# Optimization experiments

Hardware: AMD Instinct MI355X
Metric: run time of the kernel (lower is better)

The kernel has to match this reference:

```python
import jax, jax.numpy as jnp
import numpy as np
from jax import lax

L = 12  # db6 filter length
REC_LO = np.array([0.11154074335008017, 0.4946238903983854, 0.7511339080215775,
                   0.3152503517092432, -0.22626469396516913, -0.12976686756709563,
                   0.09750160558707936, 0.02752286553001629, -0.031582039318031156,
                   0.0005538422009938016, 0.004777257511010651, -0.00107730108499558])
DEC_LO = REC_LO[::-1]
_sgn = (-1.0) ** np.arange(L)
DEC_HI = -_sgn * REC_LO            # pywt dec_hi
REC_HI = _sgn * DEC_LO             # pywt rec_hi
# XLA conv = cross-correlation; pytorch_wavelets correlates with reversed dec filters
K_ANA = np.ascontiguousarray(np.stack([DEC_LO[::-1], DEC_HI[::-1]])[:, None, :])  # (2,1,12)
# conv_transpose(stride2, pad L-2) == dilate-by-2, pad 1, correlate with flipped rec filters
K_SYN = np.ascontiguousarray(np.stack([REC_LO[::-1], REC_HI[::-1]])[None, :, :])  # (1,2,12)
J = 8


def _afb(x):
    # one analysis level, symmetric mode (pytorch_wavelets afb1d)
    B, C, N = x.shape
    out = (N + L - 1) // 2
    p = 2 * (out - 1) - N + L
    xp = jnp.pad(x, ((0, 0), (0, 0), (p // 2, p - p // 2)), mode='symmetric')
    y = lax.conv_general_dilated(xp.reshape(B * C, 1, -1), jnp.asarray(K_ANA, x.dtype),
                                 (2,), 'VALID', dimension_numbers=('NCH', 'OIH', 'NCH'))
    y = y.reshape(B, C, 2, out)
    return y[:, :, 0], y[:, :, 1]


def _sfb(lo, hi):
    # one synthesis level (pytorch_wavelets sfb1d); crop lo to hi length first
    lo = lo[..., :hi.shape[-1]]
    B, C, N = lo.shape
    z = jnp.stack([lo, hi], 2).reshape(B * C, 2, N)
    y = lax.conv_general_dilated(z, jnp.asarray(K_SYN, lo.dtype), (1,), [(1, 1)],
                                 lhs_dilation=(2,), dimension_numbers=('NCH', 'OIH', 'NCH'))
    return y.reshape(B, C, -1)  # length 2N - L + 2


def _wave_conv(x, w1, w2):
    lo, highs = x, []
    for _ in range(J):
        lo, hi = _afb(lo)
        highs.append(hi)
    lo = jnp.einsum('bix,iox->box', lo, w1)
    highs[-1] = jnp.einsum('bix,iox->box', highs[-1], w2)
    for hi in highs[::-1]:
        lo = _sfb(lo, hi)
    return lo


def _branch(xg, fc0_w, fc0_b, ww1, ww2, cw, cb, fc1_w, fc1_b, fc2_w, fc2_b):
    v = jnp.transpose(xg @ fc0_w + fc0_b, (0, 2, 1))  # (B,C,S)
    for i in range(4):
        a = _wave_conv(v, ww1[i], ww2[i])
        b = jnp.einsum('bcs,oc->bos', v, cw[i]) + cb[i][None, :, None]
        v = a + b
        if i < 3:
            v = jax.nn.gelu(v, approximate=False)
    v = jnp.transpose(v, (0, 2, 1))
    v = jax.nn.gelu(v @ fc1_w + fc1_b, approximate=False)
    return v @ fc2_w + fc2_b


def setup_inputs() -> dict:
    key = jax.random.key(0)
    ks = iter(jax.random.split(key, 32))
    B, S, W, LV = 64, 1024, 64, 8
    d = {"x": jax.random.normal(next(ks), (B, S, 1), jnp.float32)}
    def params(pref):
        sc = 1.0 / (W * W)
        d[pref + "fc0_w"] = jax.random.normal(next(ks), (2, W), jnp.float32) * 0.5
        d[pref + "fc0_b"] = jax.random.normal(next(ks), (W,), jnp.float32) * 0.1
        d[pref + "wave_w1"] = sc * jax.random.uniform(next(ks), (4, W, W, LV + 6), jnp.float32)
        d[pref + "wave_w2"] = sc * jax.random.uniform(next(ks), (4, W, W, LV + 6), jnp.float32)
        d[pref + "cw"] = jax.random.normal(next(ks), (4, W, W), jnp.float32) * (1.0 / np.sqrt(W))
        d[pref + "cb"] = jax.random.normal(next(ks), (4, W), jnp.float32) * 0.05
        d[pref + "fc1_w"] = jax.random.normal(next(ks), (W, 128), jnp.float32) * (1.0 / np.sqrt(W))
        d[pref + "fc1_b"] = jax.random.normal(next(ks), (128,), jnp.float32) * 0.05
        d[pref + "fc2_w"] = jax.random.normal(next(ks), (128, 1), jnp.float32) * (1.0 / np.sqrt(128))
        d[pref + "fc2_b"] = jax.random.normal(next(ks), (1,), jnp.float32) * 0.05
    params("")
    params("nt_")
    return d


def reference(x, fc0_w, fc0_b, wave_w1, wave_w2, cw, cb, fc1_w, fc1_b, fc2_w, fc2_b,
              nt_fc0_w, nt_fc0_b, nt_wave_w1, nt_wave_w2, nt_cw, nt_cb,
              nt_fc1_w, nt_fc1_b, nt_fc2_w, nt_fc2_b):
    B, S, _ = x.shape
    grid = jnp.broadcast_to(jnp.linspace(0.0, 1.0, S, dtype=x.dtype)[None, :, None], (B, S, 1))
    xg = jnp.concatenate([x, grid], -1)
    y = _branch(xg, fc0_w, fc0_b, wave_w1, wave_w2, cw, cb, fc1_w, fc1_b, fc2_w, fc2_b)
    y_nt = _branch(xg, nt_fc0_w, nt_fc0_b, nt_wave_w1, nt_wave_w2, nt_cw, nt_cb,
                   nt_fc1_w, nt_fc1_b, nt_fc2_w, nt_fc2_b)
    return y + y_nt
```

## Files before the change

kernel.cpp:

```cpp
#include <hip/hip_runtime.h>
#include <hip/hip_bf16.h>
#include <math.h>


#define BDIM 64
#define SLEN 1024
#define WCH  64
#define BC   (BDIM*WCH)
#define NT   16

typedef short s16x8 __attribute__((ext_vector_type(8)));
typedef float f32x4 __attribute__((ext_vector_type(4)));
typedef unsigned short u16x4 __attribute__((ext_vector_type(4)));

constexpr float RLv[12] = {
    0.11154074335008017f, 0.4946238903983854f, 0.7511339080215775f,
    0.3152503517092432f, -0.22626469396516913f, -0.12976686756709563f,
    0.09750160558707936f, 0.02752286553001629f, -0.031582039318031156f,
    0.0005538422009938016f, 0.004777257511010651f, -0.00107730108499558f };
constexpr float AHv[12] = {
     RLv[11], -RLv[10],  RLv[9], -RLv[8],  RLv[7], -RLv[6],
     RLv[5],  -RLv[4],   RLv[3], -RLv[2],  RLv[1], -RLv[0] };
constexpr float SLv[12] = {
     RLv[11], RLv[10], RLv[9], RLv[8], RLv[7], RLv[6],
     RLv[5],  RLv[4],  RLv[3], RLv[2], RLv[1], RLv[0] };
constexpr float SHv[12] = {
    -RLv[0],  RLv[1], -RLv[2],  RLv[3], -RLv[4],  RLv[5],
    -RLv[6],  RLv[7], -RLv[8],  RLv[9], -RLv[10], RLv[11] };

__device__ __forceinline__ float gelu_f(float x) {
    float z = 0.7978845608f * (x + 0.044715f * x * x * x);
    return x / (1.0f + __expf(-2.0f * z));
}
__device__ __forceinline__ unsigned short f2bf(float f) {
    __hip_bfloat16 h = __float2bfloat16(f);
    union { __hip_bfloat16 h; unsigned short u; } cv; cv.h = h; return cv.u;
}
__device__ __forceinline__ float bf2f(unsigned short u) {
    union { unsigned short u; __hip_bfloat16 h; } cv; cv.u = u;
    return __bfloat162float(cv.h);
}
__device__ __forceinline__ void unpack_frag2(uint4 a, uint4 b,
                                             s16x8* ah, s16x8* al) {
    union { s16x8 v; unsigned int d[4]; } H, L;
    H.d[0] = __builtin_amdgcn_perm(a.y, a.x, 0x05040100u);
    H.d[1] = __builtin_amdgcn_perm(a.w, a.z, 0x05040100u);
    H.d[2] = __builtin_amdgcn_perm(b.y, b.x, 0x05040100u);
    H.d[3] = __builtin_amdgcn_perm(b.w, b.z, 0x05040100u);
    L.d[0] = __builtin_amdgcn_perm(a.y, a.x, 0x07060302u);
    L.d[1] = __builtin_amdgcn_perm(a.w, a.z, 0x07060302u);
    L.d[2] = __builtin_amdgcn_perm(b.y, b.x, 0x07060302u);
    L.d[3] = __builtin_amdgcn_perm(b.w, b.z, 0x07060302u);
    *ah = H.v; *al = L.v;
}

__device__ __forceinline__ int swz(int c, int s) {
    return c * 64 + ((((s >> 3) ^ (c & 7)) << 3) | (s & 7));
}
__device__ __forceinline__ int swz2(int s, int c) {
    return s * 64 + ((((c >> 3) ^ (s & 7)) << 3) | (c & 7));
}

__device__ __forceinline__ void proj2(
    const unsigned short* Phi, const unsigned short* Plo,
    const unsigned short* __restrict__ Ahi, const unsigned short* __restrict__ Alo,
    float* __restrict__ Ppart, int bb, int tile, int s0, int t)
{
    const int lane = t & 63;
    const int w    = t >> 6;
    const int qr   = lane >> 4;
    const int ln   = lane & 15;

    s16x8 pah[2][2], pal[2][2];
#pragma unroll
    for (int kk = 0; kk < 2; ++kk)
#pragma unroll
        for (int mt = 0; mt < 2; ++mt) {
            const int arow = (mt * 16 + ln) * SLEN + s0 + kk * 32 + qr * 8;
            pah[kk][mt] = *(const s16x8*)&Ahi[arow];
            pal[kk][mt] = *(const s16x8*)&Alo[arow];
        }

    f32x4 pP[2][2], pS[2][2];
#pragma unroll
    for (int mt = 0; mt < 2; ++mt)
#pragma unroll
        for (int ni = 0; ni < 2; ++ni) {
            pP[mt][ni] = (f32x4){0.f,0.f,0.f,0.f};
            pS[mt][ni] = (f32x4){0.f,0.f,0.f,0.f};
        }

#pragma unroll
    for (int kk = 0; kk < 2; ++kk) {
        const int bk = kk * 4 + qr;
#pragma unroll
        for (int ni = 0; ni < 2; ++ni) {
            const int c = w * 32 + ni * 16 + ln;
            const int boff = c * 64 + ((bk ^ (c & 7)) << 3);
            s16x8 bh = *(const s16x8*)&Phi[boff];
            s16x8 bl = *(const s16x8*)&Plo[boff];
#pragma unroll
            for (int mt = 0; mt < 2; ++mt) {
                pP[mt][ni] = __builtin_amdgcn_mfma_f32_16x16x32_bf16(pah[kk][mt], bh, pP[mt][ni], 0, 0, 0);
                pS[mt][ni] = __builtin_amdgcn_mfma_f32_16x16x32_bf16(pal[kk][mt], bh, pS[mt][ni], 0, 0, 0);
                pS[mt][ni] = __builtin_amdgcn_mfma_f32_16x16x32_bf16(pah[kk][mt], bl, pS[mt][ni], 0, 0, 0);
            }
        }
    }
#pragma unroll
    for (int mt = 0; mt < 2; ++mt)
#pragma unroll
        for (int ni = 0; ni < 2; ++ni) {
            const int c = w * 32 + ni * 16 + ln;
            f32x4 pv = pP[mt][ni] + pS[mt][ni];
#pragma unroll
            for (int r = 0; r < 4; ++r) {
                const int xr = mt * 16 + qr * 4 + r;
                if (xr < 28)
                    Ppart[((size_t)(bb * NT + tile) * 28 + xr) * 64 + c] = pv[r];
            }
        }
}

__global__ __launch_bounds__(256) void setup_kernel(
    const float* __restrict__ x,
    unsigned short* __restrict__ Ahi, unsigned short* __restrict__ Alo,
    unsigned short* __restrict__ MThi, unsigned short* __restrict__ MTlo,
    float* __restrict__ axbuf,
    const float* __restrict__ fc1w_0, const float* __restrict__ fc1w_1,
    const float* __restrict__ cw_0, const float* __restrict__ cw_1,
    const float* __restrict__ w1_0, const float* __restrict__ w2_0,
    const float* __restrict__ w1_1, const float* __restrict__ w2_1,
    unsigned short* __restrict__ w1hi, unsigned short* __restrict__ w1lo,
    unsigned short* __restrict__ cwPhi, unsigned short* __restrict__ cwPlo,
    unsigned short* __restrict__ Dhi,  unsigned short* __restrict__ Dlo,
    float* __restrict__ WsT)
{
    __shared__ float Af[1024];
    __shared__ float Bff[520];
    __shared__ float hib[14];
    const int t = threadIdx.x;

    if (blockIdx.x < 1024 || (blockIdx.x >= 1052 && blockIdx.x < 1118)) {
        const bool isA = (blockIdx.x < 1024);
        const int s0 = blockIdx.x;
        const int di = blockIdx.x - 1052;
        for (int i = t; i < SLEN; i += 256) {
            float v;
            if (isA)           v = (i == s0) ? 1.0f : 0.0f;
            else if (di < 64)  v = x[di * SLEN + i];
            else if (di == 64) v = (float)i * (1.0f / 1023.0f);
            else               v = 1.0f;
            Af[i] = v;
        }
        __syncthreads();

        const int NIN[8]  = {1024, 517, 264, 137, 74, 42, 26, 18};
        const int NOUT[8] = { 517, 264, 137,  74, 42, 26, 18, 14};
#pragma unroll
        for (int lev = 0; lev < 8; ++lev) {
            float* in  = (lev & 1) ? Bff : Af;
            float* out = (lev & 1) ? Af : Bff;
            const int nin = NIN[lev], nout = NOUT[lev];
            for (int m = t; m < nout; m += 256) {
                float alo = 0.f, ahi = 0.f;
#pragma unroll
                for (int tt = 0; tt < 12; ++tt) {
                    int jj = 2 * m + tt - 10;
                    if (jj < 0)         jj = -1 - jj;
                    else if (jj >= nin) jj = 2 * nin - 1 - jj;
                    float xv = in[jj];
                    alo += xv * RLv[tt];
                    if (lev == 7) ahi += xv * AHv[tt];
                }
                out[m] = alo;
                if (lev == 7) {
                    if (isA) {
                        unsigned short h1 = f2bf(alo);
                        Ahi[m * SLEN + s0] = h1;
                        Alo[m * SLEN + s0] = f2bf(alo - bf2f(h1));
                        unsigned short h2 = f2bf(ahi);
                        Ahi[(14 + m) * SLEN + s0] = h2;
                        Alo[(14 + m) * SLEN + s0] = f2bf(ahi - bf2f(h2));
                    } else {
                        axbuf[di * 28 + m]      = alo;
                        axbuf[di * 28 + 14 + m] = ahi;
                    }
                }
            }
            __syncthreads();
        }
        if (isA && t < 4) {
            Ahi[(28 + t) * SLEN + s0] = 0; Alo[(28 + t) * SLEN + s0] = 0;
            MThi[s0 * 32 + 28 + t] = 0;    MTlo[s0 * 32 + 28 + t] = 0;
        }
        return;
    }

    if (blockIdx.x >= 1126) {
        const int wsb = blockIdx.x - 1126;
        const int L = wsb >> 2, br = (wsb >> 1) & 1, which = wsb & 1;
        const float* src = (which ? (br ? w2_1 : w2_0) : (br ? w1_1 : w1_0))
                         + (size_t)L * 64 * 64 * 14;
        const size_t dbase = ((size_t)(L * 2 + br) * 28 + which * 14) * 4096;
        for (int e = t; e < 4096; e += 256) {
            const float* sp = src + (size_t)e * 14;
            float v[14];
#pragma unroll
            for (int xi = 0; xi < 14; ++xi) v[xi] = sp[xi];
#pragma unroll
            for (int xi = 0; xi < 14; ++xi)
                WsT[dbase + (size_t)xi * 4096 + e] = v[xi];
        }
        return;
    }

    if (blockIdx.x >= 1118) {
        const int gid = (blockIdx.x - 1118) * 256 + t;
        for (int idx = gid; idx < 16384; idx += 2048) {
            int br = idx >> 13, r = idx & 8191;
            int h = r >> 6, c = r & 63;
            float f = (br ? fc1w_1 : fc1w_0)[c * 128 + h];
            unsigned short hh = f2bf(f);
            w1hi[idx] = hh;
            w1lo[idx] = f2bf(f - bf2f(hh));
        }
        for (int idx = gid; idx < 32768; idx += 2048) {
            int L = idx >> 13, br = (idx >> 12) & 1, e = idx & 4095;
            int k = e >> 6, o = e & 63;
            float val = (br ? cw_1 : cw_0)[(size_t)L * 4096 + o * 64 + k]
                      + ((k == o) ? 1.0f : 0.0f);
            unsigned short h = f2bf(val);
            const int off = (L * 2 + br) * 4096 + o * 64 + k;
            cwPhi[off] = h;
            cwPlo[off] = f2bf(val - bf2f(h));
        }
        for (int idx = gid; idx < 32768; idx += 2048) {
            int bb = idx >> 8, o = (idx >> 2) & 63, j = idx & 3;
            Dhi[bb * 2048 + o * 32 + 28 + j] = 0;
            Dlo[bb * 2048 + o * 32 + 28 + j] = 0;
        }
        return;
    }

    const int u = blockIdx.x - 1024;
    if (t < 14) {
        Af[t]  = (u < 14 && t == u) ? 1.0f : 0.0f;
        hib[t] = (u >= 14 && t == (u - 14)) ? 1.0f : 0.0f;
    }
    __syncthreads();

    const int NH[8] = {14, 18, 26, 42, 74, 137, 264, 517};
    const int NO[8] = {18, 26, 42, 74, 138, 264, 518, 1024};

#pragma unroll
    for (int s = 0; s < 8; ++s) {
        const float* lo = (s & 1) ? Bff : Af;
        float* out      = (s & 1) ? Af : Bff;
        const int N = NH[s], nout = NO[s];
        for (int m = t; m < nout; m += 256) {
            float acc = 0.f;
#pragma unroll
            for (int tt = 0; tt < 12; ++tt) {
                int uu = m + tt - 1;
                if ((uu & 1) == 0) {
                    int q = uu >> 1;
                    if (q < N) {
                        acc += lo[q] * SLv[tt];
                        if (s == 0) acc += hib[q] * SHv[tt];
                    }
                }
            }
            out[m] = acc;
        }
        __syncthreads();
    }
    for (int m = t; m < SLEN; m += 256) {
        float f = Af[m];
        unsigned short h = f2bf(f);
        MThi[m * 32 + u] = h;
        MTlo[m * 32 + u] = f2bf(f - bf2f(h));
    }
}

__global__ __launch_bounds__(256) void mix0_kernel(
    const float* __restrict__ axbuf,
    const float* __restrict__ fc0w_0, const float* __restrict__ fc0b_0,
    const float* __restrict__ fc0w_1, const float* __restrict__ fc0b_1,
    const float* __restrict__ WsT0,
    unsigned short* __restrict__ Dhi, unsigned short* __restrict__ Dlo)
{
    const int t = threadIdx.x;
    const int br  = blockIdx.x / 224;
    const int sub = blockIdx.x % 224;

    __shared__ float Ws[64][65];
    __shared__ float LO[8][64];
    const int o = t & 63;
    const int w = t >> 6;
    const int x  = sub >> 3;
    const int b0 = (sub & 7) << 3;

    const float* wsrc = WsT0 + ((size_t)(br * 28 + x)) * 4096;
    for (int idx = t; idx < 4096; idx += 256)
        Ws[idx >> 6][idx & 63] = wsrc[idx];

    const float* fc0w = br ? fc0w_1 : fc0w_0;
    const float* fc0b = br ? fc0b_1 : fc0b_0;
    const float agv = axbuf[64 * 28 + x];
    const float a1v = axbuf[65 * 28 + x];
    const float w0o = fc0w[o];
    const float wgo = fc0w[WCH + o];
    const float b0o = fc0b[o];

#pragma unroll
    for (int j = 0; j < 2; ++j) {
        int bi = w + 4 * j;
        int b  = b0 + bi;
        float axv = axbuf[b * 28 + x];
        LO[bi][o] = axv * w0o + agv * wgo + a1v * b0o;
    }
    __syncthreads();

#pragma unroll
    for (int j = 0; j < 2; ++j) {
        int bi = w + 4 * j;
        int bb = br * 64 + b0 + bi;
        float acc = 0.f;
        for (int i = 0; i < 64; ++i)
            acc += LO[bi][i] * Ws[i][o];
        acc -= LO[bi][o];
        unsigned short h = f2bf(acc);
        Dhi[bb * 2048 + o * 32 + x] = h;
        Dlo[bb * 2048 + o * 32 + x] = f2bf(acc - bf2f(h));
    }
}

__global__ __launch_bounds__(256) void mix_kernel(
    const float* __restrict__ Ppart,
    const float* __restrict__ WsTL,
    unsigned short* __restrict__ Dhi, unsigned short* __restrict__ Dlo)
{
    const int t = threadIdx.x;
    const int br  = blockIdx.x / 224;
    const int sub = blockIdx.x % 224;

    __shared__ float Ws[64][65];
    __shared__ float LO[8][64];
    const int o = t & 63;
    const int w = t >> 6;
    const int x  = sub >> 3;
    const int b0 = (sub & 7) << 3;

    const float* wsrc = WsTL + ((size_t)(br * 28 + x)) * 4096;
    for (int idx = t; idx < 4096; idx += 256)
        Ws[idx >> 6][idx & 63] = wsrc[idx];

#pragma unroll
    for (int j = 0; j < 2; ++j) {
        int bi = w + 4 * j;
        int bb = br * 64 + b0 + bi;
        float s = 0.f;
        for (int tile = 0; tile < NT; ++tile)
            s += Ppart[((size_t)(bb * NT + tile) * 28 + x) * 64 + o];
        LO[bi][o] = s;
    }
    __syncthreads();

#pragma unroll
    for (int j = 0; j < 2; ++j) {
        int bi = w + 4 * j;
        int bb = br * 64 + b0 + bi;
        float acc = 0.f;
        for (int i = 0; i < 64; ++i)
            acc += LO[bi][i] * Ws[i][o];
        acc -= LO[bi][o];
        unsigned short h = f2bf(acc);
        Dhi[bb * 2048 + o * 32 + x] = h;
        Dlo[bb * 2048 + o * 32 + x] = f2bf(acc - bf2f(h));
    }
}

__global__ __launch_bounds__(128, 3) void layer_kernel(
    const unsigned int* __restrict__ vin0, const unsigned int* __restrict__ vin1,
    unsigned int* __restrict__ vout0, unsigned int* __restrict__ vout1,
    const unsigned short* __restrict__ MThi, const unsigned short* __restrict__ MTlo,
    const unsigned short* __restrict__ Ahi,  const unsigned short* __restrict__ Alo,
    const unsigned short* __restrict__ cwPhi, const unsigned short* __restrict__ cwPlo,
    const unsigned short* __restrict__ Dhi,   const unsigned short* __restrict__ Dlo,
    const float* __restrict__ cb_0, const float* __restrict__ cb_1,
    const float* __restrict__ fc0w_0, const float* __restrict__ fc0b_0,
    const float* __restrict__ fc0w_1, const float* __restrict__ fc0b_1,
    const float* __restrict__ xin,
    float* __restrict__ Ppart, int Lidx)
{
    __shared__ unsigned short Phi[4096];
    __shared__ unsigned short Plo[4096];

    const int t = threadIdx.x;
    const int bid = blockIdx.x;
    const int br  = bid >> 10;
    const int rem = bid & 1023;
    const int b    = rem >> 4;
    const int tile = rem & 15;
    const int s0   = tile << 6;
    const size_t bS = (size_t)b * SLEN;
    const unsigned int* vin = br ? vin1 : vin0;
    unsigned int* vout      = br ? vout1 : vout0;
    const float* cb = br ? cb_1 : cb_0;
    const float* f0w = br ? fc0w_1 : fc0w_0;
    const float* f0b = br ? fc0b_1 : fc0b_0;
    const int bb = br * 64 + b;
    const int cwbase = (Lidx * 2 + br) * 4096;

    const int lane = t & 63;
    const int w    = t >> 6;
    const int qr   = lane >> 4;
    const int ln   = lane & 15;

    s16x8 Bh[2][2], Bl[2][2];
#pragma unroll
    for (int kk = 0; kk < 2; ++kk)
#pragma unroll
        for (int ni = 0; ni < 2; ++ni) {
            const int o = w * 32 + ni * 16 + ln;
            const int boff = cwbase + o * 64 + kk * 32 + qr * 8;
            Bh[kk][ni] = *(const s16x8*)&cwPhi[boff];
            Bl[kk][ni] = *(const s16x8*)&cwPlo[boff];
        }
    s16x8 Dhf[2], Dlf[2];
#pragma unroll
    for (int ni = 0; ni < 2; ++ni) {
        const int o = w * 32 + ni * 16 + ln;
        const int boff = bb * 2048 + o * 32 + qr * 8;
        Dhf[ni] = *(const s16x8*)&Dhi[boff];
        Dlf[ni] = *(const s16x8*)&Dlo[boff];
    }
    float cbv[2];
#pragma unroll
    for (int ni = 0; ni < 2; ++ni) cbv[ni] = cb[w * 32 + ni * 16 + ln];

    uint4 vb[2][2];
    float xpf = 0.f;
    if (Lidx == 0) {
        xpf = xin[bS + s0 + ln];
    } else {
        const size_t a0 = (bS + s0 + ln) * 64 + qr * 8;
        vb[0][0] = *(const uint4*)&vin[a0];
        vb[0][1] = *(const uint4*)&vin[a0 + 4];
        vb[1][0] = *(const uint4*)&vin[a0 + 32];
        vb[1][1] = *(const uint4*)&vin[a0 + 36];
    }

#pragma unroll
    for (int mi = 0; mi < 4; ++mi) {
        const int srow = mi * 16 + ln;
        uint4 vn[2][2];
        float xnf = 0.f;
        if (mi < 3) {
            if (Lidx == 0) {
                xnf = xin[bS + s0 + (mi + 1) * 16 + ln];
            } else {
                const size_t an = (bS + s0 + (mi + 1) * 16 + ln) * 64 + qr * 8;
                vn[0][0] = *(const uint4*)&vin[an];
                vn[0][1] = *(const uint4*)&vin[an + 4];
                vn[1][0] = *(const uint4*)&vin[an + 32];
                vn[1][1] = *(const uint4*)&vin[an + 36];
            }
        }

        f32x4 accP[2], accS[2];
#pragma unroll
        for (int ni = 0; ni < 2; ++ni) {
            accP[ni] = (f32x4){0.f,0.f,0.f,0.f};
            accS[ni] = (f32x4){0.f,0.f,0.f,0.f};
        }

#pragma unroll
        for (int kk = 0; kk < 2; ++kk) {
            s16x8 ah, al;
            if (Lidx == 0) {
                const int s = s0 + srow;
                const float gv = (float)s * (1.0f / 1023.0f);
#pragma unroll
                for (int j = 0; j < 8; ++j) {
                    const int c = kk * 32 + qr * 8 + j;
                    float val = xpf * f0w[c] + gv * f0w[WCH + c] + f0b[c];
                    unsigned short h = f2bf(val);
                    ah[j] = (short)h;
                    al[j] = (short)f2bf(val - bf2f(h));
                }
            } else {
                unpack_frag2(vb[kk][0], vb[kk][1], &ah, &al);
            }
#pragma unroll
            for (int ni = 0; ni < 2; ++ni) {
                accP[ni] = __builtin_amdgcn_mfma_f32_16x16x32_bf16(ah, Bh[kk][ni], accP[ni], 0, 0, 0);
                accS[ni] = __builtin_amdgcn_mfma_f32_16x16x32_bf16(al, Bh[kk][ni], accS[ni], 0, 0, 0);
                accS[ni] = __builtin_amdgcn_mfma_f32_16x16x32_bf16(ah, Bl[kk][ni], accS[ni], 0, 0, 0);
            }
        }
        {
            const size_t aoff = (size_t)(s0 + srow) * 32 + qr * 8;
            s16x8 mh = *(const s16x8*)&MThi[aoff];
            s16x8 ml = *(const s16x8*)&MTlo[aoff];
#pragma unroll
            for (int ni = 0; ni < 2; ++ni) {
                accP[ni] = __builtin_amdgcn_mfma_f32_16x16x32_bf16(mh, Dhf[ni], accP[ni], 0, 0, 0);
                accS[ni] = __builtin_amdgcn_mfma_f32_16x16x32_bf16(ml, Dhf[ni], accS[ni], 0, 0, 0);
                accS[ni] = __builtin_amdgcn_mfma_f32_16x16x32_bf16(mh, Dlf[ni], accS[ni], 0, 0, 0);
            }
        }
#pragma unroll
        for (int ni = 0; ni < 2; ++ni) {
            const int o = w * 32 + ni * 16 + ln;
            f32x4 acc = accP[ni] + accS[ni];
            u16x4 hv, lv;
#pragma unroll
            for (int r = 0; r < 4; ++r) {
                const int sl64 = mi * 16 + qr * 4 + r;
                float val = gelu_f(acc[r] + cbv[ni]);
                unsigned short h = f2bf(val);
                unsigned short l = f2bf(val - bf2f(h));
                vout[(bS + s0 + sl64) * 64 + o] =
                    (unsigned int)h | ((unsigned int)l << 16);
                hv[r] = h;
                lv[r] = l;
            }
            const int a = swz(o, mi * 16 + qr * 4);
            *(u16x4*)&Phi[a] = hv;
            *(u16x4*)&Plo[a] = lv;
        }
        if (mi < 3) {
            if (Lidx == 0) {
                xpf = xnf;
            } else {
                vb[0][0] = vn[0][0]; vb[0][1] = vn[0][1];
                vb[1][0] = vn[1][0]; vb[1][1] = vn[1][1];
            }
        }
    }

    proj2(Phi, Plo, Ahi, Alo, Ppart, bb, tile, s0, t);
}

__global__ __launch_bounds__(256, 2) void head_kernel(
    const unsigned int* __restrict__ vin0, const unsigned int* __restrict__ vin1,
    const unsigned short* __restrict__ MThi, const unsigned short* __restrict__ MTlo,
    const unsigned short* __restrict__ cwPhi, const unsigned short* __restrict__ cwPlo,
    const unsigned short* __restrict__ Dhi,   const unsigned short* __restrict__ Dlo,
    const float* __restrict__ cb_0, const float* __restrict__ cb_1,
    const unsigned short* __restrict__ w1hi, const unsigned short* __restrict__ w1lo,
    const float* __restrict__ fc1b_0, const float* __restrict__ fc2w_0,
    const float* __restrict__ fc2b_0,
    const float* __restrict__ fc1b_1, const float* __restrict__ fc2w_1,
    const float* __restrict__ fc2b_1,
    float* __restrict__ out)
{
    __shared__ unsigned short Vh[8192];
    __shared__ unsigned short Vl[8192];
    __shared__ float SP[4][64];

    const int t = threadIdx.x;
    const int bid = blockIdx.x;
    const int b    = bid >> 4;
    const int tile = bid & 15;
    const int s0   = tile << 6;
    const size_t bS = (size_t)b * SLEN;

    const int lane = t & 63;
    const int w    = t >> 6;
    const int br   = w >> 1;
    const int half = w & 1;
    const int qr   = lane >> 4;
    const int ln   = lane & 15;

    const unsigned int* vin = br ? vin1 : vin0;
    const float* cb   = (br ? cb_1 : cb_0) + 3 * WCH;
    const float* fc1b = br ? fc1b_1 : fc1b_0;
    const float* fc2w = br ? fc2w_1 : fc2w_0;
    const int bb = br * 64 + b;
    const int cwbase = (3 * 2 + br) * 4096;
    unsigned short* Vhp = Vh + br * 4096;
    unsigned short* Vlp = Vl + br * 4096;

    {
        s16x8 Bh[2][2], Bl[2][2];
#pragma unroll
        for (int kk = 0; kk < 2; ++kk)
#pragma unroll
            for (int ni = 0; ni < 2; ++ni) {
                const int o = half * 32 + ni * 16 + ln;
                const int boff = cwbase + o * 64 + kk * 32 + qr * 8;
                Bh[kk][ni] = *(const s16x8*)&cwPhi[boff];
                Bl[kk][ni] = *(const s16x8*)&cwPlo[boff];
            }
        s16x8 Dhf[2], Dlf[2];
#pragma unroll
        for (int ni = 0; ni < 2; ++ni) {
            const int o = half * 32 + ni * 16 + ln;
            const int boff = bb * 2048 + o * 32 + qr * 8;
            Dhf[ni] = *(const s16x8*)&Dhi[boff];
            Dlf[ni] = *(const s16x8*)&Dlo[boff];
        }
        float cbv[2];
#pragma unroll
        for (int ni = 0; ni < 2; ++ni) cbv[ni] = cb[half * 32 + ni * 16 + ln];

        uint4 vb[2][2];
        {
            const size_t a0 = (bS + s0 + ln) * 64 + qr * 8;
            vb[0][0] = *(const uint4*)&vin[a0];
            vb[0][1] = *(const uint4*)&vin[a0 + 4];
            vb[1][0] = *(const uint4*)&vin[a0 + 32];
            vb[1][1] = *(const uint4*)&vin[a0 + 36];
        }

#pragma unroll
        for (int mi = 0; mi < 4; ++mi) {
            uint4 vn[2][2];
            if (mi < 3) {
                const size_t an = (bS + s0 + (mi + 1) * 16 + ln) * 64 + qr * 8;
                vn[0][0] = *(const uint4*)&vin[an];
                vn[0][1] = *(const uint4*)&vin[an + 4];
                vn[1][0] = *(const uint4*)&vin[an + 32];
                vn[1][1] = *(const uint4*)&vin[an + 36];
            }
            const int srow = mi * 16 + ln;
            f32x4 accP[2], accS[2];
#pragma unroll
            for (int ni = 0; ni < 2; ++ni) {
                accP[ni] = (f32x4){0.f,0.f,0.f,0.f};
                accS[ni] = (f32x4){0.f,0.f,0.f,0.f};
            }

#pragma unroll
            for (int kk = 0; kk < 2; ++kk) {
                s16x8 ah, al;
                unpack_frag2(vb[kk][0], vb[kk][1], &ah, &al);
#pragma unroll
                for (int ni = 0; ni < 2; ++ni) {
                    accP[ni] = __builtin_amdgcn_mfma_f32_16x16x32_bf16(ah, Bh[kk][ni], accP[ni], 0, 0, 0);
                    accS[ni] = __builtin_amdgcn_mfma_f32_16x16x32_bf16(al, Bh[kk][ni], accS[ni], 0, 0, 0);
                    accS[ni] = __builtin_amdgcn_mfma_f32_16x16x32_bf16(ah, Bl[kk][ni], accS[ni], 0, 0, 0);
                }
            }
            {
                const size_t aoff = (size_t)(s0 + srow) * 32 + qr * 8;
                s16x8 mh = *(const s16x8*)&MThi[aoff];
                s16x8 ml = *(const s16x8*)&MTlo[aoff];
#pragma unroll
                for (int ni = 0; ni < 2; ++ni) {
                    accP[ni] = __builtin_amdgcn_mfma_f32_16x16x32_bf16(mh, Dhf[ni], accP[ni], 0, 0, 0);
                    accS[ni] = __builtin_amdgcn_mfma_f32_16x16x32_bf16(ml, Dhf[ni], accS[ni], 0, 0, 0);
                    accS[ni] = __builtin_amdgcn_mfma_f32_16x16x32_bf16(mh, Dlf[ni], accS[ni], 0, 0, 0);
                }
            }
#pragma unroll
            for (int ni = 0; ni < 2; ++ni) {
                const int o = half * 32 + ni * 16 + ln;
                f32x4 acc = accP[ni] + accS[ni];
#pragma unroll
                for (int r = 0; r < 4; ++r) {
                    const int sl64 = mi * 16 + qr * 4 + r;
                    float val = acc[r] + cbv[ni];
                    unsigned short h = f2bf(val);
                    unsigned short l = f2bf(val - bf2f(h));
                    const int a = swz2(sl64, o);
                    Vhp[a] = h;
                    Vlp[a] = l;
                }
            }
            if (mi < 3) {
                vb[0][0] = vn[0][0]; vb[0][1] = vn[0][1];
                vb[1][0] = vn[1][0]; vb[1][1] = vn[1][1];
            }
        }
    }
    __syncthreads();

    s16x8 Wh[2][4], Wl[2][4];
#pragma unroll
    for (int kk = 0; kk < 2; ++kk)
#pragma unroll
        for (int ni = 0; ni < 4; ++ni) {
            const int h = half * 64 + ni * 16 + ln;
            const int boff = br * 8192 + h * 64 + kk * 32 + qr * 8;
            Wh[kk][ni] = *(const s16x8*)&w1hi[boff];
            Wl[kk][ni] = *(const s16x8*)&w1lo[boff];
        }
    float b1v[4], w2v[4];
#pragma unroll
    for (int ni = 0; ni < 4; ++ni) {
        b1v[ni] = fc1b[half * 64 + ni * 16 + ln];
        w2v[ni] = fc2w[half * 64 + ni * 16 + ln];
    }

#pragma unroll
    for (int mi = 0; mi < 4; ++mi) {
        f32x4 a1P[4], a1S[4];
#pragma unroll
        for (int ni = 0; ni < 4; ++ni) {
            a1P[ni] = (f32x4){0.f,0.f,0.f,0.f};
            a1S[ni] = (f32x4){0.f,0.f,0.f,0.f};
        }

#pragma unroll
        for (int kk = 0; kk < 2; ++kk) {
            const int blk = kk * 4 + qr;
            const int sl  = mi * 16 + ln;
            const int a   = sl * 64 + ((blk ^ (sl & 7)) << 3);
            s16x8 ah = *(const s16x8*)&Vhp[a];
            s16x8 al = *(const s16x8*)&Vlp[a];
#pragma unroll
            for (int ni = 0; ni < 4; ++ni) {
                a1P[ni] = __builtin_amdgcn_mfma_f32_16x16x32_bf16(ah, Wh[kk][ni], a1P[ni], 0, 0, 0);
                a1S[ni] = __builtin_amdgcn_mfma_f32_16x16x32_bf16(al, Wh[kk][ni], a1S[ni], 0, 0, 0);
                a1S[ni] = __builtin_amdgcn_mfma_f32_16x16x32_bf16(ah, Wl[kk][ni], a1S[ni], 0, 0, 0);
            }
        }
        float partial[4] = {0.f, 0.f, 0.f, 0.f};
#pragma unroll
        for (int ni = 0; ni < 4; ++ni) {
            f32x4 acc1 = a1P[ni] + a1S[ni];
#pragma unroll
            for (int r = 0; r < 4; ++r)
                partial[r] += gelu_f(acc1[r] + b1v[ni]) * w2v[ni];
        }
#pragma unroll
        for (int r = 0; r < 4; ++r) {
            partial[r] += __shfl_xor(partial[r], 1, 64);
            partial[r] += __shfl_xor(partial[r], 2, 64);
            partial[r] += __shfl_xor(partial[r], 4, 64);
            partial[r] += __shfl_xor(partial[r], 8, 64);
        }
        if (ln == 0) {
#pragma unroll
            for (int r = 0; r < 4; ++r)
                SP[w][mi * 16 + qr * 4 + r] = partial[r];
        }
    }
    __syncthreads();

    if (t < 64) {
        const float bias = fc2b_0[0] + fc2b_1[0];
        out[bS + s0 + t] = SP[0][t] + SP[1][t] + SP[2][t] + SP[3][t] + bias;
    }
}

extern "C" void kernel_launch(void* const* d_in, const int* in_sizes, int n_in,
                              void* d_out, int out_size, void* d_ws, size_t ws_size,
                              hipStream_t stream)
{
    const float* x = (const float*)d_in[0];
    const float* P[2][10];
    for (int br = 0; br < 2; ++br)
        for (int k = 0; k < 10; ++k)
            P[br][k] = (const float*)d_in[1 + br * 10 + k];

    char* p = (char*)d_ws;
    const size_t PL = (size_t)BC * SLEN * 4;
    unsigned int* vplane[4];
    for (int i = 0; i < 4; ++i) { vplane[i] = (unsigned int*)p; p += PL; }
    unsigned short* Ahi  = (unsigned short*)p; p += 32 * SLEN * 2;
    unsigned short* Alo  = (unsigned short*)p; p += 32 * SLEN * 2;
    unsigned short* MThi = (unsigned short*)p; p += SLEN * 32 * 2;
    unsigned short* MTlo = (unsigned short*)p; p += SLEN * 32 * 2;
    float* Ppart = (float*)p;                  p += (size_t)128 * NT * 28 * 64 * 4;
    unsigned short* cwPhi = (unsigned short*)p; p += 8 * 4096 * 2;
    unsigned short* cwPlo = (unsigned short*)p; p += 8 * 4096 * 2;
    unsigned short* Dhi   = (unsigned short*)p; p += (size_t)128 * 2048 * 2;
    unsigned short* Dlo   = (unsigned short*)p; p += (size_t)128 * 2048 * 2;
    unsigned short* w1hi  = (unsigned short*)p; p += 2 * 8192 * 2;
    unsigned short* w1lo  = (unsigned short*)p; p += 2 * 8192 * 2;
    float* axbuf          = (float*)p;          p += 66 * 28 * 4;
    float* WsT            = (float*)p;          p += (size_t)4 * 2 * 28 * 4096 * 4;

    unsigned int *v0a = vplane[0], *v0b = vplane[1];
    unsigned int *v1a = vplane[2], *v1b = vplane[3];

    setup_kernel<<<1142, 256, 0, stream>>>(
        x, Ahi, Alo, MThi, MTlo, axbuf,
        P[0][6], P[1][6], P[0][4], P[1][4],
        P[0][2], P[0][3], P[1][2], P[1][3],
        w1hi, w1lo, cwPhi, cwPlo, Dhi, Dlo, WsT);

    mix0_kernel<<<448, 256, 0, stream>>>(
        axbuf, P[0][0], P[0][1], P[1][0], P[1][1],
        WsT, Dhi, Dlo);

    for (int i = 0; i < 3; ++i) {
        layer_kernel<<<2048, 128, 0, stream>>>(
            v0a, v1a, v0b, v1b,
            MThi, MTlo, Ahi, Alo, cwPhi, cwPlo, Dhi, Dlo,
            P[0][5] + (size_t)i * WCH, P[1][5] + (size_t)i * WCH,
            P[0][0], P[0][1], P[1][0], P[1][1], x,
            Ppart, i);
        unsigned int* tmp;
        tmp = v0a; v0a = v0b; v0b = tmp;
        tmp = v1a; v1a = v1b; v1b = tmp;

        mix_kernel<<<448, 256, 0, stream>>>(
            Ppart,
            WsT + (size_t)(i + 1) * 2 * 28 * 4096,
            Dhi, Dlo);
    }

    head_kernel<<<1024, 256, 0, stream>>>(
        v0a, v1a,
        MThi, MTlo, cwPhi, cwPlo, Dhi, Dlo,
        P[0][5] + (size_t)3 * WCH, P[1][5] + (size_t)3 * WCH,
        w1hi, w1lo,
        P[0][7], P[0][8], P[0][9],
        P[1][7], P[1][8], P[1][9],
        (float*)d_out);
}
```

Measured before the change: 252.8 us.

## Fuse mix stage into layer kernel via atomic accumulation and per-batch counters

```diff
diff --git a/kernel.cpp b/kernel.cpp
--- a/kernel.cpp
+++ b/kernel.cpp
@@ -7,7 +7,6 @@
 #define SLEN 1024
 #define WCH  64
 #define BC   (BDIM*WCH)
-#define NT   16
 
 typedef short s16x8 __attribute__((ext_vector_type(8)));
 typedef float f32x4 __attribute__((ext_vector_type(4)));
@@ -61,10 +60,10 @@
     return s * 64 + ((((c >> 3) ^ (s & 7)) << 3) | (c & 7));
 }
 
-__device__ __forceinline__ void proj2(
+__device__ __forceinline__ void proj2_acc(
     const unsigned short* Phi, const unsigned short* Plo,
     const unsigned short* __restrict__ Ahi, const unsigned short* __restrict__ Alo,
-    float* __restrict__ Ppart, int bb, int tile, int s0, int t)
+    float* __restrict__ LOacc, int bb, int s0, int t)
 {
     const int lane = t & 63;
     const int w    = t >> 6;
@@ -117,7 +116,7 @@
             for (int r = 0; r < 4; ++r) {
                 const int xr = mt * 16 + qr * 4 + r;
                 if (xr < 28)
-                    Ppart[((size_t)(bb * NT + tile) * 28 + xr) * 64 + c] = pv[r];
+                    unsafeAtomicAdd(&LOacc[((size_t)bb * 28 + xr) * 64 + c], pv[r]);
             }
         }
 }
@@ -134,7 +133,8 @@
     unsigned short* __restrict__ w1hi, unsigned short* __restrict__ w1lo,
     unsigned short* __restrict__ cwPhi, unsigned short* __restrict__ cwPlo,
     unsigned short* __restrict__ Dhi,  unsigned short* __restrict__ Dlo,
-    float* __restrict__ WsT)
+    float* __restrict__ WsT,
+    float* __restrict__ LOacc, int* __restrict__ ctr)
 {
     __shared__ float Af[1024];
     __shared__ float Bff[520];
@@ -240,6 +240,10 @@
             Dhi[bb * 2048 + o * 32 + 28 + j] = 0;
             Dlo[bb * 2048 + o * 32 + 28 + j] = 0;
         }
+        for (int idx = gid; idx < 3 * 128 * 28 * 64; idx += 2048)
+            LOacc[idx] = 0.f;
+        for (int idx = gid; idx < 3 * 128; idx += 2048)
+            ctr[idx] = 0;
         return;
     }
 
@@ -336,69 +340,73 @@
     }
 }
 
-__global__ __launch_bounds__(256) void mix_kernel(
-    const float* __restrict__ Ppart,
-    const float* __restrict__ WsTL,
-    unsigned short* __restrict__ Dhi, unsigned short* __restrict__ Dlo)
-{
-    const int t = threadIdx.x;
-    const int br  = blockIdx.x / 224;
-    const int sub = blockIdx.x % 224;
-
-    __shared__ float Ws[64][65];
-    __shared__ float LO[8][64];
-    const int o = t & 63;
-    const int w = t >> 6;
-    const int x  = sub >> 3;
-    const int b0 = (sub & 7) << 3;
-
-    const float* wsrc = WsTL + ((size_t)(br * 28 + x)) * 4096;
-    for (int idx = t; idx < 4096; idx += 256)
-        Ws[idx >> 6][idx & 63] = wsrc[idx];
-
-#pragma unroll
-    for (int j = 0; j < 2; ++j) {
-        int bi = w + 4 * j;
-        int bb = br * 64 + b0 + bi;
-        float s = 0.f;
-        for (int tile = 0; tile < NT; ++tile)
-            s += Ppart[((size_t)(bb * NT + tile) * 28 + x) * 64 + o];
-        LO[bi][o] = s;
-    }
-    __syncthreads();
-
-#pragma unroll
-    for (int j = 0; j < 2; ++j) {
-        int bi = w + 4 * j;
-        int bb = br * 64 + b0 + bi;
-        float acc = 0.f;
-        for (int i = 0; i < 64; ++i)
-            acc += LO[bi][i] * Ws[i][o];
-        acc -= LO[bi][o];
-        unsigned short h = f2bf(acc);
-        Dhi[bb * 2048 + o * 32 + x] = h;
-        Dlo[bb * 2048 + o * 32 + x] = f2bf(acc - bf2f(h));
-    }
-}
-
-__global__ __launch_bounds__(128, 3) void layer_kernel(
+__global__ __launch_bounds__(128, 3) void fused_kernel(
     const unsigned int* __restrict__ vin0, const unsigned int* __restrict__ vin1,
     unsigned int* __restrict__ vout0, unsigned int* __restrict__ vout1,
     const unsigned short* __restrict__ MThi, const unsigned short* __restrict__ MTlo,
     const unsigned short* __restrict__ Ahi,  const unsigned short* __restrict__ Alo,
     const unsigned short* __restrict__ cwPhi, const unsigned short* __restrict__ cwPlo,
-    const unsigned short* __restrict__ Dhi,   const unsigned short* __restrict__ Dlo,
+    unsigned short* __restrict__ Dhi,   unsigned short* __restrict__ Dlo,
     const float* __restrict__ cb_0, const float* __restrict__ cb_1,
     const float* __restrict__ fc0w_0, const float* __restrict__ fc0b_0,
     const float* __restrict__ fc0w_1, const float* __restrict__ fc0b_1,
     const float* __restrict__ xin,
-    float* __restrict__ Ppart, int Lidx)
+    float* __restrict__ LOacc, int* __restrict__ ctr,
+    const float* __restrict__ WsTnext, int Lidx)
 {
-    __shared__ unsigned short Phi[4096];
-    __shared__ unsigned short Plo[4096];
-
+    __shared__ __align__(16) char smem[64*65*4 + 8*64*4];
     const int t = threadIdx.x;
     const int bid = blockIdx.x;
+
+    if (bid >= 2048) {
+        float* Ws  = (float*)smem;
+        float* LOs = (float*)(smem + 64 * 65 * 4);
+        const int mb  = bid - 2048;
+        const int br  = mb / 224;
+        const int sub = mb % 224;
+        const int x   = sub >> 3;
+        const int b0  = (sub & 7) << 3;
+        const int bbase = br * 64 + b0;
+
+        const float* wsrc = WsTnext + ((size_t)(br * 28 + x)) * 4096;
+        for (int idx = t; idx < 4096; idx += 128)
+            Ws[(idx >> 6) * 65 + (idx & 63)] = wsrc[idx];
+
+        if (t < 8) {
+            int* cp = &ctr[bbase + t];
+            while (__hip_atomic_load(cp, __ATOMIC_ACQUIRE,
+                                     __HIP_MEMORY_SCOPE_AGENT) < 16)
+                __builtin_amdgcn_s_sleep(8);
+        }
+        __syncthreads();
+        __threadfence();
+
+        for (int e = t; e < 512; e += 128) {
+            const int bi = e >> 6, c = e & 63;
+            LOs[bi * 64 + c] = LOacc[((size_t)(bbase + bi) * 28 + x) * 64 + c];
+        }
+        __syncthreads();
+
+        const int o = t & 63;
+        const int w = t >> 6;
+#pragma unroll
+        for (int j = 0; j < 4; ++j) {
+            const int bi = w * 4 + j;
+            const int bb = bbase + bi;
+            float acc = 0.f;
+            for (int i = 0; i < 64; ++i)
+                acc += LOs[bi * 64 + i] * Ws[i * 65 + o];
+            acc -= LOs[bi * 64 + o];
+            unsigned short h = f2bf(acc);
+            Dhi[bb * 2048 + o * 32 + x] = h;
+            Dlo[bb * 2048 + o * 32 + x] = f2bf(acc - bf2f(h));
+        }
+        return;
+    }
+
+    unsigned short* Phi = (unsigned short*)smem;
+    unsigned short* Plo = (unsigned short*)(smem + 8192);
+
     const int br  = bid >> 10;
     const int rem = bid & 1023;
     const int b    = rem >> 4;
@@ -541,7 +549,13 @@
         }
     }
 
-    proj2(Phi, Plo, Ahi, Alo, Ppart, bb, tile, s0, t);
+    proj2_acc(Phi, Plo, Ahi, Alo, LOacc, bb, s0, t);
+
+    __threadfence();
+    __syncthreads();
+    if (t == 0)
+        __hip_atomic_fetch_add(&ctr[bb], 1, __ATOMIC_RELEASE,
+                               __HIP_MEMORY_SCOPE_AGENT);
 }
 
 __global__ __launch_bounds__(256, 2) void head_kernel(
@@ -766,7 +780,6 @@
     unsigned short* Alo  = (unsigned short*)p; p += 32 * SLEN * 2;
     unsigned short* MThi = (unsigned short*)p; p += SLEN * 32 * 2;
     unsigned short* MTlo = (unsigned short*)p; p += SLEN * 32 * 2;
-    float* Ppart = (float*)p;                  p += (size_t)128 * NT * 28 * 64 * 4;
     unsigned short* cwPhi = (unsigned short*)p; p += 8 * 4096 * 2;
     unsigned short* cwPlo = (unsigned short*)p; p += 8 * 4096 * 2;
     unsigned short* Dhi   = (unsigned short*)p; p += (size_t)128 * 2048 * 2;
@@ -775,6 +788,8 @@
     unsigned short* w1lo  = (unsigned short*)p; p += 2 * 8192 * 2;
     float* axbuf          = (float*)p;          p += 66 * 28 * 4;
     float* WsT            = (float*)p;          p += (size_t)4 * 2 * 28 * 4096 * 4;
+    float* LOacc          = (float*)p;          p += (size_t)3 * 128 * 28 * 64 * 4;
+    int*   ctr            = (int*)p;            p += 3 * 128 * 4;
 
     unsigned int *v0a = vplane[0], *v0b = vplane[1];
     unsigned int *v1a = vplane[2], *v1b = vplane[3];
@@ -783,27 +798,25 @@
         x, Ahi, Alo, MThi, MTlo, axbuf,
         P[0][6], P[1][6], P[0][4], P[1][4],
         P[0][2], P[0][3], P[1][2], P[1][3],
-        w1hi, w1lo, cwPhi, cwPlo, Dhi, Dlo, WsT);
+        w1hi, w1lo, cwPhi, cwPlo, Dhi, Dlo, WsT, LOacc, ctr);
 
     mix0_kernel<<<448, 256, 0, stream>>>(
         axbuf, P[0][0], P[0][1], P[1][0], P[1][1],
         WsT, Dhi, Dlo);
 
     for (int i = 0; i < 3; ++i) {
-        layer_kernel<<<2048, 128, 0, stream>>>(
+        fused_kernel<<<2496, 128, 0, stream>>>(
             v0a, v1a, v0b, v1b,
             MThi, MTlo, Ahi, Alo, cwPhi, cwPlo, Dhi, Dlo,
             P[0][5] + (size_t)i * WCH, P[1][5] + (size_t)i * WCH,
             P[0][0], P[0][1], P[1][0], P[1][1], x,
-            Ppart, i);
+            LOacc + (size_t)i * 128 * 28 * 64,
+            ctr + i * 128,
+            WsT + (size_t)(i + 1) * 2 * 28 * 4096,
+            i);
         unsigned int* tmp;
         tmp = v0a; v0a = v0b; v0b = tmp;
         tmp = v1a; v1a = v1b; v1b = tmp;
-
-        mix_kernel<<<448, 256, 0, stream>>>(
-            Ppart,
-            WsT + (size_t)(i + 1) * 2 * 28 * 4096,
-            Dhi, Dlo);
     }
 
     head_kernel<<<1024, 256, 0, stream>>>(
```

Measured after the change: 943.0 us. +272.9%, slower.

## Halve layer_kernel sequence tile to 32 and double grid, dropping software prefetch

Applied to the files above, without the earlier changes.

```diff
diff --git a/kernel.cpp b/kernel.cpp
--- a/kernel.cpp
+++ b/kernel.cpp
@@ -7,7 +7,7 @@
 #define SLEN 1024
 #define WCH  64
 #define BC   (BDIM*WCH)
-#define NT   16
+#define NT2  32
 
 typedef short s16x8 __attribute__((ext_vector_type(8)));
 typedef float f32x4 __attribute__((ext_vector_type(4)));
@@ -54,72 +54,11 @@
     *ah = H.v; *al = L.v;
 }
 
-__device__ __forceinline__ int swz(int c, int s) {
-    return c * 64 + ((((s >> 3) ^ (c & 7)) << 3) | (s & 7));
+__device__ __forceinline__ int swz32(int c, int s) {
+    return c * 32 + ((((s >> 3) ^ (c & 3)) << 3) | (s & 7));
 }
 __device__ __forceinline__ int swz2(int s, int c) {
     return s * 64 + ((((c >> 3) ^ (s & 7)) << 3) | (c & 7));
-}
-
-__device__ __forceinline__ void proj2(
-    const unsigned short* Phi, const unsigned short* Plo,
-    const unsigned short* __restrict__ Ahi, const unsigned short* __restrict__ Alo,
-    float* __restrict__ Ppart, int bb, int tile, int s0, int t)
-{
-    const int lane = t & 63;
-    const int w    = t >> 6;
-    const int qr   = lane >> 4;
-    const int ln   = lane & 15;
-
-    s16x8 pah[2][2], pal[2][2];
-#pragma unroll
-    for (int kk = 0; kk < 2; ++kk)
-#pragma unroll
-        for (int mt = 0; mt < 2; ++mt) {
-            const int arow = (mt * 16 + ln) * SLEN + s0 + kk * 32 + qr * 8;
-            pah[kk][mt] = *(const s16x8*)&Ahi[arow];
-            pal[kk][mt] = *(const s16x8*)&Alo[arow];
-        }
-
-    f32x4 pP[2][2], pS[2][2];
-#pragma unroll
-    for (int mt = 0; mt < 2; ++mt)
-#pragma unroll
-        for (int ni = 0; ni < 2; ++ni) {
-            pP[mt][ni] = (f32x4){0.f,0.f,0.f,0.f};
-            pS[mt][ni] = (f32x4){0.f,0.f,0.f,0.f};
-        }
-
-#pragma unroll
-    for (int kk = 0; kk < 2; ++kk) {
-        const int bk = kk * 4 + qr;
-#pragma unroll
-        for (int ni = 0; ni < 2; ++ni) {
-            const int c = w * 32 + ni * 16 + ln;
-            const int boff = c * 64 + ((bk ^ (c & 7)) << 3);
-            s16x8 bh = *(const s16x8*)&Phi[boff];
-            s16x8 bl = *(const s16x8*)&Plo[boff];
-#pragma unroll
-            for (int mt = 0; mt < 2; ++mt) {
-                pP[mt][ni] = __builtin_amdgcn_mfma_f32_16x16x32_bf16(pah[kk][mt], bh, pP[mt][ni], 0, 0, 0);
-                pS[mt][ni] = __builtin_amdgcn_mfma_f32_16x16x32_bf16(pal[kk][mt], bh, pS[mt][ni], 0, 0, 0);
-                pS[mt][ni] = __builtin_amdgcn_mfma_f32_16x16x32_bf16(pah[kk][mt], bl, pS[mt][ni], 0, 0, 0);
-            }
-        }
-    }
-#pragma unroll
-    for (int mt = 0; mt < 2; ++mt)
-#pragma unroll
-        for (int ni = 0; ni < 2; ++ni) {
-            const int c = w * 32 + ni * 16 + ln;
-            f32x4 pv = pP[mt][ni] + pS[mt][ni];
-#pragma unroll
-            for (int r = 0; r < 4; ++r) {
-                const int xr = mt * 16 + qr * 4 + r;
-                if (xr < 28)
-                    Ppart[((size_t)(bb * NT + tile) * 28 + xr) * 64 + c] = pv[r];
-            }
-        }
 }
 
 __global__ __launch_bounds__(256) void setup_kernel(
@@ -361,8 +300,8 @@
         int bi = w + 4 * j;
         int bb = br * 64 + b0 + bi;
         float s = 0.f;
-        for (int tile = 0; tile < NT; ++tile)
-            s += Ppart[((size_t)(bb * NT + tile) * 28 + x) * 64 + o];
+        for (int tp = 0; tp < NT2; ++tp)
+            s += Ppart[((size_t)(bb * NT2 + tp) * 28 + x) * 64 + o];
         LO[bi][o] = s;
     }
     __syncthreads();
@@ -394,16 +333,16 @@
     const float* __restrict__ xin,
     float* __restrict__ Ppart, int Lidx)
 {
-    __shared__ unsigned short Phi[4096];
-    __shared__ unsigned short Plo[4096];
+    __shared__ unsigned short Phi[2048];
+    __shared__ unsigned short Plo[2048];
 
     const int t = threadIdx.x;
     const int bid = blockIdx.x;
-    const int br  = bid >> 10;
-    const int rem = bid & 1023;
-    const int b    = rem >> 4;
-    const int tile = rem & 15;
-    const int s0   = tile << 6;
+    const int br  = bid >> 11;
+    const int rem = bid & 2047;
+    const int b    = rem >> 5;
+    const int t32  = rem & 31;
+    const int s0   = t32 << 5;
     const size_t bS = (size_t)b * SLEN;
     const unsigned int* vin = br ? vin1 : vin0;
     unsigned int* vout      = br ? vout1 : vout0;
@@ -440,35 +379,9 @@
 #pragma unroll
     for (int ni = 0; ni < 2; ++ni) cbv[ni] = cb[w * 32 + ni * 16 + ln];
 
-    uint4 vb[2][2];
-    float xpf = 0.f;
-    if (Lidx == 0) {
-        xpf = xin[bS + s0 + ln];
-    } else {
-        const size_t a0 = (bS + s0 + ln) * 64 + qr * 8;
-        vb[0][0] = *(const uint4*)&vin[a0];
-        vb[0][1] = *(const uint4*)&vin[a0 + 4];
-        vb[1][0] = *(const uint4*)&vin[a0 + 32];
-        vb[1][1] = *(const uint4*)&vin[a0 + 36];
-    }
-
-#pragma unroll
-    for (int mi = 0; mi < 4; ++mi) {
+#pragma unroll
+    for (int mi = 0; mi < 2; ++mi) {
         const int srow = mi * 16 + ln;
-        uint4 vn[2][2];
-        float xnf = 0.f;
-        if (mi < 3) {
-            if (Lidx == 0) {
-                xnf = xin[bS + s0 + (mi + 1) * 16 + ln];
-            } else {
-                const size_t an = (bS + s0 + (mi + 1) * 16 + ln) * 64 + qr * 8;
-                vn[0][0] = *(const uint4*)&vin[an];
-                vn[0][1] = *(const uint4*)&vin[an + 4];
-                vn[1][0] = *(const uint4*)&vin[an + 32];
-                vn[1][1] = *(const uint4*)&vin[an + 36];
-            }
-        }
-
         f32x4 accP[2], accS[2];
 #pragma unroll
         for (int ni = 0; ni < 2; ++ni) {
@@ -481,17 +394,21 @@
             s16x8 ah, al;
             if (Lidx == 0) {
                 const int s = s0 + srow;
+                const float xv = xin[bS + s];
                 const float gv = (float)s * (1.0f / 1023.0f);
 #pragma unroll
                 for (int j = 0; j < 8; ++j) {
                     const int c = kk * 32 + qr * 8 + j;
-                    float val = xpf * f0w[c] + gv * f0w[WCH + c] + f0b[c];
+                    float val = xv * f0w[c] + gv * f0w[WCH + c] + f0b[c];
                     unsigned short h = f2bf(val);
                     ah[j] = (short)h;
                     al[j] = (short)f2bf(val - bf2f(h));
                 }
             } else {
-                unpack_frag2(vb[kk][0], vb[kk][1], &ah, &al);
+                const size_t aoff = (bS + s0 + srow) * 64 + kk * 32 + qr * 8;
+                uint4 va = *(const uint4*)&vin[aoff];
+                uint4 vbq = *(const uint4*)&vin[aoff + 4];
+                unpack_frag2(va, vbq, &ah, &al);
             }
 #pragma unroll
             for (int ni = 0; ni < 2; ++ni) {
@@ -518,30 +435,64 @@
             u16x4 hv, lv;
 #pragma unroll
             for (int r = 0; r < 4; ++r) {
-                const int sl64 = mi * 16 + qr * 4 + r;
+                const int sl32 = mi * 16 + qr * 4 + r;
                 float val = gelu_f(acc[r] + cbv[ni]);
                 unsigned short h = f2bf(val);
                 unsigned short l = f2bf(val - bf2f(h));
-                vout[(bS + s0 + sl64) * 64 + o] =
+                vout[(bS + s0 + sl32) * 64 + o] =
                     (unsigned int)h | ((unsigned int)l << 16);
                 hv[r] = h;
                 lv[r] = l;
             }
-            const int a = swz(o, mi * 16 + qr * 4);
+            const int a = swz32(o, mi * 16 + qr * 4);
             *(u16x4*)&Phi[a] = hv;
             *(u16x4*)&Plo[a] = lv;
         }
-        if (mi < 3) {
-            if (Lidx == 0) {
-                xpf = xnf;
-            } else {
-                vb[0][0] = vn[0][0]; vb[0][1] = vn[0][1];
-                vb[1][0] = vn[1][0]; vb[1][1] = vn[1][1];
-            }
-        }
-    }
-
-    proj2(Phi, Plo, Ahi, Alo, Ppart, bb, tile, s0, t);
+    }
+
+    {
+        s16x8 pah[2], pal[2];
+#pragma unroll
+        for (int mt = 0; mt < 2; ++mt) {
+            const int arow = (mt * 16 + ln) * SLEN + s0 + qr * 8;
+            pah[mt] = *(const s16x8*)&Ahi[arow];
+            pal[mt] = *(const s16x8*)&Alo[arow];
+        }
+        f32x4 pP[2][2], pS[2][2];
+#pragma unroll
+        for (int mt = 0; mt < 2; ++mt)
+#pragma unroll
+            for (int ni = 0; ni < 2; ++ni) {
+                pP[mt][ni] = (f32x4){0.f,0.f,0.f,0.f};
+                pS[mt][ni] = (f32x4){0.f,0.f,0.f,0.f};
+            }
+#pragma unroll
+        for (int ni = 0; ni < 2; ++ni) {
+            const int c = w * 32 + ni * 16 + ln;
+            const int boff = c * 32 + ((qr ^ (c & 3)) << 3);
+            s16x8 bh = *(const s16x8*)&Phi[boff];
+            s16x8 bl = *(const s16x8*)&Plo[boff];
+#pragma unroll
+            for (int mt = 0; mt < 2; ++mt) {
+                pP[mt][ni] = __builtin_amdgcn_mfma_f32_16x16x32_bf16(pah[mt], bh, pP[mt][ni], 0, 0, 0);
+                pS[mt][ni] = __builtin_amdgcn_mfma_f32_16x16x32_bf16(pal[mt], bh, pS[mt][ni], 0, 0, 0);
+                pS[mt][ni] = __builtin_amdgcn_mfma_f32_16x16x32_bf16(pah[mt], bl, pS[mt][ni], 0, 0, 0);
+            }
+        }
+#pragma unroll
+        for (int mt = 0; mt < 2; ++mt)
+#pragma unroll
+            for (int ni = 0; ni < 2; ++ni) {
+                const int c = w * 32 + ni * 16 + ln;
+                f32x4 pv = pP[mt][ni] + pS[mt][ni];
+#pragma unroll
+                for (int r = 0; r < 4; ++r) {
+                    const int xr = mt * 16 + qr * 4 + r;
+                    if (xr < 28)
+                        Ppart[((size_t)(bb * NT2 + t32) * 28 + xr) * 64 + c] = pv[r];
+                }
+            }
+    }
 }
 
 __global__ __launch_bounds__(256, 2) void head_kernel(
@@ -766,7 +717,7 @@
     unsigned short* Alo  = (unsigned short*)p; p += 32 * SLEN * 2;
     unsigned short* MThi = (unsigned short*)p; p += SLEN * 32 * 2;
     unsigned short* MTlo = (unsigned short*)p; p += SLEN * 32 * 2;
-    float* Ppart = (float*)p;                  p += (size_t)128 * NT * 28 * 64 * 4;
+    float* Ppart = (float*)p;                  p += (size_t)128 * NT2 * 28 * 64 * 4;
     unsigned short* cwPhi = (unsigned short*)p; p += 8 * 4096 * 2;
     unsigned short* cwPlo = (unsigned short*)p; p += 8 * 4096 * 2;
     unsigned short* Dhi   = (unsigned short*)p; p += (size_t)128 * 2048 * 2;
@@ -790,7 +741,7 @@
         WsT, Dhi, Dlo);
 
     for (int i = 0; i < 3; ++i) {
-        layer_kernel<<<2048, 128, 0, stream>>>(
+        layer_kernel<<<4096, 128, 0, stream>>>(
             v0a, v1a, v0b, v1b,
             MThi, MTlo, Ahi, Alo, cwPhi, cwPlo, Dhi, Dlo,
             P[0][5] + (size_t)i * WCH, P[1][5] + (size_t)i * WCH,
```

After: 266.9 us. 5.5% more time.
